# Performance work log

Hardware: AMD Instinct MI355X
Metric: run time of the kernel (lower is better)

Reference implementation:

```python
import jax, jax.numpy as jnp
import numpy as np

BLOCK_SIZE = 3
SOBEL_PAD = 1  # sobel_size // 2
BLOCK_PAD = BLOCK_SIZE // 2

_SOBEL_X = jnp.array([[-1.0, 0.0, 1.0], [-2.0, 0.0, 2.0], [-1.0, 0.0, 1.0]], dtype=jnp.float32)[None, None]
_SOBEL_Y = jnp.array([[-1.0, -2.0, -1.0], [0.0, 0.0, 0.0], [1.0, 2.0, 1.0]], dtype=jnp.float32)[None, None]
_SUM_K = jnp.ones((1, 1, BLOCK_SIZE, BLOCK_SIZE), dtype=jnp.float32)


def _pad_replicate(x, p):
    return jnp.pad(x, ((0, 0), (0, 0), (p, p), (p, p)), mode='edge')


def _conv(x, k):
    return jax.lax.conv_general_dilated(
        x, k, window_strides=(1, 1), padding='VALID',
        dimension_numbers=('NCHW', 'OIHW', 'NCHW'))


def setup_inputs() -> dict:
    key = jax.random.key(0)
    image = jax.random.uniform(key, (8, 1, 1080, 1920), dtype=jnp.float32) * 255.0
    return {"image": image}


def reference(image) -> jnp.ndarray:
    img = image.astype(jnp.float32)
    img_p = _pad_replicate(img, SOBEL_PAD)
    Ix = _conv(img_p, _SOBEL_X)
    Iy = _conv(img_p, _SOBEL_Y)
    Ixx = Ix * Ix
    Iyy = Iy * Iy
    Ixy = Ix * Iy
    sum_Ixx = _conv(_pad_replicate(Ixx, BLOCK_PAD), _SUM_K)
    sum_Iyy = _conv(_pad_replicate(Iyy, BLOCK_PAD), _SUM_K)
    sum_Ixy = _conv(_pad_replicate(Ixy, BLOCK_PAD), _SUM_K)
    half_trace = (sum_Ixx + sum_Iyy) * 0.5
    diff_half = (sum_Ixx - sum_Iyy) * 0.5
    sqrt_disc = jnp.sqrt(diff_half * diff_half + sum_Ixy * sum_Ixy + 1e-10)
    lambda_min = half_trace - sqrt_disc
    return jnp.clip(lambda_min, 0.0)
```

## Files before the change

kernel.cpp:

```cpp
#include <hip/hip_runtime.h>

#define IMG_H 1080
#define IMG_W 1920
#define NBATCH 8

struct __attribute__((aligned(8))) f4u { float a, b, c, d; };

__global__ __launch_bounds__(256, 3)
void shi_tomasi_kernel(const float* __restrict__ img, float* __restrict__ out) {
    const int cg    = threadIdx.x & 31;
    const int strip = threadIdx.x >> 5;
    const int vb = blockIdx.x * 128 + cg * 4;
    const int s0 = blockIdx.y * 72 + strip * 9;
    const int b  = blockIdx.z;
    const float* g = img + (size_t)b * (IMG_H * IMG_W);

    const bool eL = (vb == 0);
    const bool eR = (vb == IMG_W - 4);
    const int  o0 = eL ? 0 : (eR ? vb - 4 : vb - 2);
    const bool topFix = (s0 == 0);
    const bool botFix = (s0 + 9 == IMG_H);

    float raw[5][8];
    float hdR[3][6], hsR[3][6], hfd[3], hfs[3], h[3][12];

    auto issue = [&](int k) {
        int lr = s0 - 2 + k; lr = max(0, min(IMG_H - 1, lr));
        const float* rp = g + (size_t)lr * IMG_W + o0;
        const f4u va = *(const f4u*)rp;
        const f4u vc = *(const f4u*)(rp + 4);
        float* r = raw[k % 5];
        r[0] = va.a; r[1] = va.b; r[2] = va.c; r[3] = va.d;
        r[4] = vc.a; r[5] = vc.b; r[6] = vc.c; r[7] = vc.d;
    };

    #pragma unroll
    for (int k = 0; k < 4; ++k) issue(k);

    float* orow = out + ((size_t)b * IMG_H + s0) * IMG_W + vb;

    #pragma unroll
    for (int k = 0; k < 13; ++k) {
        if (k + 4 < 13) issue(k + 4);

        {
            const float* r = raw[k % 5];
            float z0=r[0], z1=r[1], z2=r[2], z3=r[3], z4=r[4], z5=r[5], z6=r[6], z7=r[7];
            if (eL) { z7=z5; z6=z4; z5=z3; z4=z2; z3=z1; z2=z0; z1=z0; }
            if (eR) { z0=z2; z1=z3; z2=z4; z3=z5; z4=z6; z5=z7; z6=z7; }
            float* hd = hdR[k % 3];
            float* hs = hsR[k % 3];
            hd[0]=z2-z0; hd[1]=z3-z1; hd[2]=z4-z2; hd[3]=z5-z3; hd[4]=z6-z4; hd[5]=z7-z5;
            hs[0]=z0+2.0f*z1+z2; hs[1]=z1+2.0f*z2+z3; hs[2]=z2+2.0f*z3+z4;
            hs[3]=z3+2.0f*z4+z5; hs[4]=z4+2.0f*z5+z6; hs[5]=z5+2.0f*z6+z7;
            hfd[k % 3] = eR ? (z5-z4) : (z3-z2);
            hfs[k % 3] = eR ? (z4+3.0f*z5) : (3.0f*z2+z3);
        }

        if (k >= 2) {
            const int rr = k - 2;
            const int sm = rr % 3;
            const int sz = (rr + 1) % 3;
            const int sp = (rr + 2) % 3;

            float Ix[6], Iy[6];
            #pragma unroll
            for (int t = 0; t < 6; ++t) {
                Ix[t] = hdR[sm][t] + 2.0f * hdR[sz][t] + hdR[sp][t];
                Iy[t] = hsR[sp][t] - hsR[sm][t];
            }
            const float ixf = hfd[sm] + 2.0f * hfd[sz] + hfd[sp];
            const float iyf = hfs[sp] - hfs[sm];
            if (eL) { Ix[0] = ixf; Iy[0] = iyf; }
            if (eR) { Ix[5] = ixf; Iy[5] = iyf; }

            float pxx[6], pyy[6], pxy[6];
            #pragma unroll
            for (int t = 0; t < 6; ++t) {
                pxx[t] = Ix[t] * Ix[t];
                pyy[t] = Iy[t] * Iy[t];
                pxy[t] = Ix[t] * Iy[t];
            }
            float* hr = h[rr % 3];
            #pragma unroll
            for (int o = 0; o < 4; ++o) {
                hr[o]     = pxx[o] + pxx[o+1] + pxx[o+2];
                hr[4 + o] = pyy[o] + pyy[o+1] + pyy[o+2];
                hr[8 + o] = pxy[o] + pxy[o+1] + pxy[o+2];
            }
            if (rr == 1) {
                #pragma unroll
                for (int q = 0; q < 12; ++q) if (topFix) h[0][q] = hr[q];
            }
            if (rr == 10) {
                const float* hprev = h[(rr - 1) % 3];
                #pragma unroll
                for (int q = 0; q < 12; ++q) if (botFix) hr[q] = hprev[q];
            }

            if (rr >= 2) {
                const float* h0 = h[(rr - 2) % 3];
                const float* h1 = h[(rr - 1) % 3];
                const float* h2 = hr;
                float rv[4];
                #pragma unroll
                for (int o = 0; o < 4; ++o) {
                    const float sxx = h0[o]     + h1[o]     + h2[o];
                    const float syy = h0[4 + o] + h1[4 + o] + h2[4 + o];
                    const float sxy = h0[8 + o] + h1[8 + o] + h2[8 + o];
                    const float ht   = 0.5f * (sxx + syy);
                    const float dh   = 0.5f * (sxx - syy);
                    const float disc = fmaf(dh, dh, fmaf(sxy, sxy, 1e-10f));
                    rv[o] = fmaxf(ht - sqrtf(disc), 0.0f);
                }
                *(float4*)orow = make_float4(rv[0], rv[1], rv[2], rv[3]);
                orow += IMG_W;
            }
        }
    }
}

extern "C" void kernel_launch(void* const* d_in, const int* in_sizes, int n_in,
                              void* d_out, int out_size, void* d_ws, size_t ws_size,
                              hipStream_t stream) {
    const float* img = (const float*)d_in[0];
    float* out = (float*)d_out;
    dim3 grid(IMG_W / 128, IMG_H / 72, NBATCH);
    shi_tomasi_kernel<<<grid, 256, 0, stream>>>(img, out);
}
```

Measured before the change: 121.9 us.

## Use taller per-thread strips, aligned float4 loads, and edge-specialized templated body

Each thread now processes 15 output rows instead of 9, which cuts the share of redundant halo rows loaded per strip. Loads are now three aligned float4 reads starting at vb-4 instead of two 8-byte-aligned reads. Interior blocks run a template instance with all edge handling compiled out. The block shape becomes 64 columns by 4 strips with 8 blocks across the width, so the last block has idle threads (1920 is not a multiple of 256). Registers grow with the 12-wide raw buffer and longer unrolled loop.

```diff
diff --git a/kernel.cpp b/kernel.cpp
--- a/kernel.cpp
+++ b/kernel.cpp
@@ -3,65 +3,70 @@
 #define IMG_H 1080
 #define IMG_W 1920
 #define NBATCH 8
+#define LSTRIP 15
+#define BROWS (4*LSTRIP)
+#define NK (LSTRIP+4)
 
-struct __attribute__((aligned(8))) f4u { float a, b, c, d; };
 
-__global__ __launch_bounds__(256, 3)
-void shi_tomasi_kernel(const float* __restrict__ img, float* __restrict__ out) {
-    const int cg    = threadIdx.x & 31;
-    const int strip = threadIdx.x >> 5;
-    const int vb = blockIdx.x * 128 + cg * 4;
-    const int s0 = blockIdx.y * 72 + strip * 9;
-    const int b  = blockIdx.z;
-    const float* g = img + (size_t)b * (IMG_H * IMG_W);
+template<bool EDGE>
+__device__ __forceinline__ void st_body(const float* __restrict__ g,
+                                        float* __restrict__ orow,
+                                        int vb, int s0) {
+    const bool eL = EDGE && (vb == 0);
+    const bool eR = EDGE && (vb == IMG_W - 4);
+    int wb = vb - 4;
+    if (EDGE) { if (eL) wb = 0; if (eR) wb = IMG_W - 12; }
+    const bool topFix = (s0 == 0);
+    const bool botFix = (s0 + LSTRIP == IMG_H);
 
-    const bool eL = (vb == 0);
-    const bool eR = (vb == IMG_W - 4);
-    const int  o0 = eL ? 0 : (eR ? vb - 4 : vb - 2);
-    const bool topFix = (s0 == 0);
-    const bool botFix = (s0 + 9 == IMG_H);
-
-    float raw[5][8];
+    float raw[5][12];
     float hdR[3][6], hsR[3][6], hfd[3], hfs[3], h[3][12];
 
     auto issue = [&](int k) {
-        int lr = s0 - 2 + k; lr = max(0, min(IMG_H - 1, lr));
-        const float* rp = g + (size_t)lr * IMG_W + o0;
-        const f4u va = *(const f4u*)rp;
-        const f4u vc = *(const f4u*)(rp + 4);
+        int lr = s0 - 2 + k;
+        lr = max(0, min(IMG_H - 1, lr));
+        const float4* rp = (const float4*)(g + (size_t)lr * IMG_W + wb);
+        const float4 a = rp[0], b2 = rp[1], c = rp[2];
         float* r = raw[k % 5];
-        r[0] = va.a; r[1] = va.b; r[2] = va.c; r[3] = va.d;
-        r[4] = vc.a; r[5] = vc.b; r[6] = vc.c; r[7] = vc.d;
+        r[0]=a.x;  r[1]=a.y;  r[2]=a.z;  r[3]=a.w;
+        r[4]=b2.x; r[5]=b2.y; r[6]=b2.z; r[7]=b2.w;
+        r[8]=c.x;  r[9]=c.y;  r[10]=c.z; r[11]=c.w;
     };
 
     #pragma unroll
     for (int k = 0; k < 4; ++k) issue(k);
 
-    float* orow = out + ((size_t)b * IMG_H + s0) * IMG_W + vb;
-
     #pragma unroll
-    for (int k = 0; k < 13; ++k) {
-        if (k + 4 < 13) issue(k + 4);
+    for (int k = 0; k < NK; ++k) {
+        if (k + 4 < NK) issue(k + 4);
 
         {
             const float* r = raw[k % 5];
-            float z0=r[0], z1=r[1], z2=r[2], z3=r[3], z4=r[4], z5=r[5], z6=r[6], z7=r[7];
-            if (eL) { z7=z5; z6=z4; z5=z3; z4=z2; z3=z1; z2=z0; z1=z0; }
-            if (eR) { z0=z2; z1=z3; z2=z4; z3=z5; z4=z6; z5=z7; z6=z7; }
+            float z[8];
+            if (EDGE) {
+                const float zL[8] = {r[0],r[0],r[0],r[1],r[2],r[3],r[4],r[5]};
+                const float zR[8] = {r[6],r[7],r[8],r[9],r[10],r[11],r[11],r[11]};
+                #pragma unroll
+                for (int j = 0; j < 8; ++j)
+                    z[j] = eL ? zL[j] : (eR ? zR[j] : r[j + 2]);
+                hfd[k % 3] = eR ? (z[5] - z[4]) : (z[3] - z[2]);
+                hfs[k % 3] = eR ? (z[4] + 3.0f * z[5]) : (3.0f * z[2] + z[3]);
+            } else {
+                #pragma unroll
+                for (int j = 0; j < 8; ++j) z[j] = r[j + 2];
+            }
             float* hd = hdR[k % 3];
             float* hs = hsR[k % 3];
-            hd[0]=z2-z0; hd[1]=z3-z1; hd[2]=z4-z2; hd[3]=z5-z3; hd[4]=z6-z4; hd[5]=z7-z5;
-            hs[0]=z0+2.0f*z1+z2; hs[1]=z1+2.0f*z2+z3; hs[2]=z2+2.0f*z3+z4;
-            hs[3]=z3+2.0f*z4+z5; hs[4]=z4+2.0f*z5+z6; hs[5]=z5+2.0f*z6+z7;
-            hfd[k % 3] = eR ? (z5-z4) : (z3-z2);
-            hfs[k % 3] = eR ? (z4+3.0f*z5) : (3.0f*z2+z3);
+            #pragma unroll
+            for (int t = 0; t < 6; ++t) {
+                hd[t] = z[t + 2] - z[t];
+                hs[t] = fmaf(2.0f, z[t + 1], z[t]) + z[t + 2];
+            }
         }
 
         if (k >= 2) {
             const int rr = k - 2;
-            const int sm = rr % 3;
-            const int sz = (rr + 1) % 3;
-            const int sp = (rr + 2) % 3;
+            const int sm = rr % 3, sz = (rr + 1) % 3, sp = (rr + 2) % 3;
 
             float Ix[6], Iy[6];
             #pragma unroll
@@ -69,10 +74,12 @@
                 Ix[t] = hdR[sm][t] + 2.0f * hdR[sz][t] + hdR[sp][t];
                 Iy[t] = hsR[sp][t] - hsR[sm][t];
             }
-            const float ixf = hfd[sm] + 2.0f * hfd[sz] + hfd[sp];
-            const float iyf = hfs[sp] - hfs[sm];
-            if (eL) { Ix[0] = ixf; Iy[0] = iyf; }
-            if (eR) { Ix[5] = ixf; Iy[5] = iyf; }
+            if (EDGE) {
+                const float ixf = hfd[sm] + 2.0f * hfd[sz] + hfd[sp];
+                const float iyf = hfs[sp] - hfs[sm];
+                if (eL) { Ix[0] = ixf; Iy[0] = iyf; }
+                if (eR) { Ix[5] = ixf; Iy[5] = iyf; }
+            }
 
             float pxx[6], pyy[6], pxy[6];
             #pragma unroll
@@ -88,14 +95,14 @@
                 hr[4 + o] = pyy[o] + pyy[o+1] + pyy[o+2];
                 hr[8 + o] = pxy[o] + pxy[o+1] + pxy[o+2];
             }
-            if (rr == 1) {
+            if (rr == 1 && topFix) {
                 #pragma unroll
-                for (int q = 0; q < 12; ++q) if (topFix) h[0][q] = hr[q];
+                for (int q = 0; q < 12; ++q) h[0][q] = hr[q];
             }
-            if (rr == 10) {
+            if (rr == LSTRIP + 1 && botFix) {
                 const float* hprev = h[(rr - 1) % 3];
                 #pragma unroll
-                for (int q = 0; q < 12; ++q) if (botFix) hr[q] = hprev[q];
+                for (int q = 0; q < 12; ++q) hr[q] = hprev[q];
             }
 
             if (rr >= 2) {
@@ -120,11 +127,27 @@
     }
 }
 
+__global__ __launch_bounds__(256, 3)
+void shi_tomasi_kernel(const float* __restrict__ img, float* __restrict__ out) {
+    const int cg    = threadIdx.x & 63;
+    const int strip = threadIdx.x >> 6;
+    const int vb = blockIdx.x * 256 + cg * 4;
+    if (vb >= IMG_W) return;
+    const int s0 = blockIdx.y * BROWS + strip * LSTRIP;
+    const float* g = img + (size_t)blockIdx.z * (IMG_H * IMG_W);
+    float* orow = out + ((size_t)blockIdx.z * IMG_H + s0) * IMG_W + vb;
+
+    if (blockIdx.x == 0 || blockIdx.x == gridDim.x - 1)
+        st_body<true>(g, orow, vb, s0);
+    else
+        st_body<false>(g, orow, vb, s0);
+}
+
 extern "C" void kernel_launch(void* const* d_in, const int* in_sizes, int n_in,
                               void* d_out, int out_size, void* d_ws, size_t ws_size,
                               hipStream_t stream) {
     const float* img = (const float*)d_in[0];
     float* out = (float*)d_out;
-    dim3 grid(IMG_W / 128, IMG_H / 72, NBATCH);
+    dim3 grid(8, IMG_H / BROWS, NBATCH);
     shi_tomasi_kernel<<<grid, 256, 0, stream>>>(img, out);
 }
```

After: 126.9 us. 1.04x slower.
